# Performance work log

Measured on AMD Instinct MI355X. Metric: run time of the kernel, lower is better.

Reference implementation:

```python
import jax, jax.numpy as jnp
import numpy as np

# AdEx constants (from source module)
T_REF = 2e-3
CM = 281e-12
GL = 30e-9
EL = -70.6e-3
VT = -50.4e-3
DELTAT = 2e-3
TAUW = 144e-3
A = 4e-9
B = 0.0805e-9
DT = 1e-3
REF_STEPS = int(round(T_REF / DT))  # 2 steps


def setup_inputs() -> dict:
    key = jax.random.key(0)
    T, N = 500, 100000
    # input current ~ nanoamps so a fraction of neurons spike
    I = jax.random.normal(key, (T, N), dtype=jnp.float32) * 0.5e-9 + 0.5e-9
    v0 = jnp.full((N,), EL, dtype=jnp.float32)      # membrane potential at rest
    c0 = jnp.zeros((N,), dtype=jnp.float32)         # adaptation variable
    ref0 = jnp.zeros((N,), dtype=jnp.int32)         # refractory counters
    return {"I": I, "v0": v0, "c0": c0, "ref0": ref0}


def reference(I, v0, c0, ref0):
    """AdEx neuron simulation: scan over T timesteps, [N] state vectors.
    Returns v_trace of shape [T, N]."""

    def step(carry, I_t):
        v, c, ref = carry
        in_ref = ref > 0
        # refractory neurons are clamped to EL (tf.where(ref_op, EL, v))
        v_eff = jnp.where(in_ref, EL, v)
        # AdEx membrane dynamics (forward Euler); exp arg clipped for safety
        exp_term = GL * DELTAT * jnp.exp(jnp.minimum((v_eff - VT) / DELTAT, 15.0))
        dv = (DT / CM) * (-GL * (v_eff - EL) + exp_term - c + I_t)
        v_new = jnp.where(in_ref, EL, v_eff + dv)
        # adaptation current dynamics
        c_new = c + (DT / TAUW) * (A * (v_eff - EL) - c)
        # spike detection + reset
        spike = v_new >= VT
        v_out = jnp.where(spike, EL, v_new)
        c_out = jnp.where(spike, c_new + B, c_new)
        ref_new = jnp.where(spike, REF_STEPS, jnp.maximum(ref - 1, 0))
        return (v_out, c_out, ref_new), v_out

    (_, _, _), v_trace = jax.lax.scan(step, (v0, c0, ref0), I)
    return v_trace
```

## Files before the change

kernel.cpp:

```cpp
#include <hip/hip_runtime.h>


#define DEPTH 12

__global__ __launch_bounds__(64) void adex_kernel(
    const float* __restrict__ I,
    const float* __restrict__ v0,
    const float* __restrict__ c0,
    const int*   __restrict__ ref0,
    float*       __restrict__ out,
    int N, int T)
{
#pragma clang fp contract(off)
    const float EL       = (float)(-70.6e-3);
    const float VT       = (float)(-50.4e-3);
    const float DELTAT   = (float)(2e-3);
    const float R_DELTAT = (float)(1.0 / (double)((float)(2e-3)));
    const float NEG_GL   = (float)(-30e-9);
    const float GLDT     = (float)(30e-9 * 2e-3);
    const float DT_CM    = (float)(1e-3 / 281e-12);
    const float DT_TAUW  = (float)(1e-3 / 144e-3);
    const float Af       = (float)(4e-9);
    const float Bf       = (float)(0.0805e-9);
    const int   REF_STEPS = 2;

    int n = blockIdx.x * blockDim.x + threadIdx.x;
    if (n >= N) return;

    float v  = v0[n];
    float c  = c0[n];
    int   rf = ref0[n];

    const unsigned stride_b = (unsigned)N * 4u;
    unsigned load_off  = (unsigned)n * 4u;
    unsigned store_off = load_off;

    auto ld = [&](unsigned off) -> float {
        return *(const float*)((const char*)I + off);
    };
    auto st = [&](unsigned off, float val) {
        __builtin_nontemporal_store(val, (float*)((char*)out + off));
    };

    auto step = [&](float It) -> float {
        bool  in_ref = rf > 0;
        float v_eff  = in_ref ? EL : v;

        float x   = v_eff - VT;
        float y0  = x * R_DELTAT;
        float e   = fmaf(-DELTAT, y0, x);
        float arg = fmaf(e, R_DELTAT, y0);
        arg = fminf(arg, 15.0f);
        float exp_term = GLDT * expf(arg);

        float acc = NEG_GL * (v_eff - EL);
        acc = acc + exp_term;
        acc = acc - c;
        acc = acc + It;
        float dv = DT_CM * acc;

        float v_new = in_ref ? EL : (v_eff + dv);
        float c_new = c + DT_TAUW * ((Af * (v_eff - EL)) - c);

        bool  spike = v_new >= VT;
        float v_out = spike ? EL : v_new;

        c  = spike ? (c_new + Bf) : c_new;
        rf = spike ? REF_STEPS : (in_ref ? rf - 1 : 0);
        v  = v_out;
        return v_out;
    };

    float buf[DEPTH];

#pragma unroll
    for (int k = 0; k < DEPTH; ++k) {
        if (k < T) { buf[k] = ld(load_off); load_off += stride_b; }
    }

    int t = 0;
    for (; t + 2 * DEPTH <= T; t += DEPTH) {
#pragma unroll
        for (int j = 0; j < DEPTH; ++j) {
            float It = buf[j];
            buf[j] = ld(load_off); load_off += stride_b;
            float v_out = step(It);
            st(store_off, v_out);
            store_off += stride_b;
        }
    }

#pragma unroll
    for (int j = 0; j < 2 * DEPTH; ++j) {
        if (t + j < T) {
            float It = buf[j % DEPTH];
            if (t + j + DEPTH < T) { buf[j % DEPTH] = ld(load_off); load_off += stride_b; }
            float v_out = step(It);
            st(store_off, v_out);
            store_off += stride_b;
        }
    }
}

extern "C" void kernel_launch(void* const* d_in, const int* in_sizes, int n_in,
                              void* d_out, int out_size, void* d_ws, size_t ws_size,
                              hipStream_t stream) {
    const float* I    = (const float*)d_in[0];
    const float* v0   = (const float*)d_in[1];
    const float* c0   = (const float*)d_in[2];
    const int*   ref0 = (const int*)d_in[3];
    float*       out  = (float*)d_out;

    int N = in_sizes[1];
    int T = in_sizes[0] / N;

    dim3 block(64);
    dim3 grid((N + 63) / 64);
    adex_kernel<<<grid, block, 0, stream>>>(I, v0, c0, ref0, out, N, T);
}
```

Measured before the change: 346.8 us.

## Deepen input prefetch to 24 and share one offset for loads and stores

Doubles the register prefetch ring of input currents from 12 to 24 timesteps, keeping more loads in flight per thread to hide memory latency in the sequential scan. It also folds the separate load and store offsets into one offset, using a base pointer pre-shifted by DEPTH rows, which saves address registers and adds. A simple fallback loop handles T below 2*DEPTH. The larger buffer raises register use, though with 64-thread blocks occupancy is unlikely to be limited by it.

```diff
diff --git a/kernel.cpp b/kernel.cpp
--- a/kernel.cpp
+++ b/kernel.cpp
@@ -1,7 +1,7 @@
 #include <hip/hip_runtime.h>
 
 
-#define DEPTH 12
+#define DEPTH 24
 
 __global__ __launch_bounds__(64) void adex_kernel(
     const float* __restrict__ I,
@@ -32,15 +32,6 @@
     int   rf = ref0[n];
 
     const unsigned stride_b = (unsigned)N * 4u;
-    unsigned load_off  = (unsigned)n * 4u;
-    unsigned store_off = load_off;
-
-    auto ld = [&](unsigned off) -> float {
-        return *(const float*)((const char*)I + off);
-    };
-    auto st = [&](unsigned off, float val) {
-        __builtin_nontemporal_store(val, (float*)((char*)out + off));
-    };
 
     auto step = [&](float It) -> float {
         bool  in_ref = rf > 0;
@@ -71,33 +62,51 @@
         return v_out;
     };
 
-    float buf[DEPTH];
+    unsigned off = (unsigned)n * 4u;
+
+    if (T >= 2 * DEPTH) {
+        const char* Ip = (const char*)I + (size_t)DEPTH * (size_t)stride_b;
+
+        float buf[DEPTH];
+        {
+            unsigned poff = off;
+#pragma unroll
+            for (int k = 0; k < DEPTH; ++k) {
+                buf[k] = *(const float*)((const char*)I + poff);
+                poff += stride_b;
+            }
+        }
+
+        int t = 0;
+        for (; t + 2 * DEPTH <= T; t += DEPTH) {
+#pragma unroll
+            for (int j = 0; j < DEPTH; ++j) {
+                float It = buf[j];
+                buf[j] = *(const float*)(Ip + off);
+                float v_out = step(It);
+                __builtin_nontemporal_store(v_out, (float*)((char*)out + off));
+                off += stride_b;
+            }
+        }
 
 #pragma unroll
-    for (int k = 0; k < DEPTH; ++k) {
-        if (k < T) { buf[k] = ld(load_off); load_off += stride_b; }
-    }
-
-    int t = 0;
-    for (; t + 2 * DEPTH <= T; t += DEPTH) {
-#pragma unroll
-        for (int j = 0; j < DEPTH; ++j) {
-            float It = buf[j];
-            buf[j] = ld(load_off); load_off += stride_b;
+        for (int j = 0; j < 2 * DEPTH; ++j) {
+            if (t + j < T) {
+                float It = buf[j % DEPTH];
+                if (t + j + DEPTH < T) {
+                    buf[j % DEPTH] = *(const float*)(Ip + off);
+                }
+                float v_out = step(It);
+                __builtin_nontemporal_store(v_out, (float*)((char*)out + off));
+                off += stride_b;
+            }
+        }
+    } else {
+        for (int tt = 0; tt < T; ++tt) {
+            float It = *(const float*)((const char*)I + off);
             float v_out = step(It);
-            st(store_off, v_out);
-            store_off += stride_b;
-        }
-    }
-
-#pragma unroll
-    for (int j = 0; j < 2 * DEPTH; ++j) {
-        if (t + j < T) {
-            float It = buf[j % DEPTH];
-            if (t + j + DEPTH < T) { buf[j % DEPTH] = ld(load_off); load_off += stride_b; }
-            float v_out = step(It);
-            st(store_off, v_out);
-            store_off += stride_b;
+            __builtin_nontemporal_store(v_out, (float*)((char*)out + off));
+            off += stride_b;
         }
     }
 }
```

New measurement: 363.7 us. +4.9%, slower.
